# Kernel tuning notes

Measured on AMD Instinct MI355X. Metric: run time of the kernel, lower is better.

The kernel has to match this reference:

```python
import math
import jax, jax.numpy as jnp
import numpy as np

D_MODEL = 512
NHEAD = 8
D_HEAD = D_MODEL // NHEAD
ATTN_TEMP = 1.0
B, LQ, LK = 2, 2048, 4096


def _linear_params(key, d_in, d_out):
    kw, kb = jax.random.split(key)
    bound = 1.0 / math.sqrt(d_in)
    W = jax.random.uniform(kw, (d_out, d_in), jnp.float32, -bound, bound)
    b = jax.random.uniform(kb, (d_out,), jnp.float32, -bound, bound)
    return W, b


def setup_inputs() -> dict:
    key = jax.random.key(0)
    ks = jax.random.split(key, 8)
    q = jax.random.normal(ks[0], (B, LQ, D_MODEL), jnp.float32)
    kv = jax.random.normal(ks[1], (B, LK, D_MODEL), jnp.float32)
    key_gate = jax.random.uniform(ks[2], (B, LK), jnp.float32)
    key_mask = jax.random.randint(ks[3], (B, LK), 0, 2, jnp.int32)
    Wq, bq = _linear_params(ks[4], D_MODEL, D_MODEL)
    Wk, bk = _linear_params(ks[5], D_MODEL, D_MODEL)
    Wv, bv = _linear_params(ks[6], D_MODEL, D_MODEL)
    Wo, bo = _linear_params(ks[7], D_MODEL, D_MODEL)
    return {"q": q, "kv": kv, "key_gate": key_gate, "key_mask": key_mask,
            "Wq": Wq, "bq": bq, "Wk": Wk, "bk": bk,
            "Wv": Wv, "bv": bv, "Wo": Wo, "bo": bo}


def reference(q, kv, key_gate, key_mask, Wq, bq, Wk, bk, Wv, bv, Wo, bo):
    Bq, Lq, _ = q.shape
    _, Lk, _ = kv.shape
    # projections -> (B, H, L, Dh)
    qp = (q @ Wq.T + bq).reshape(Bq, Lq, NHEAD, D_HEAD).transpose(0, 2, 1, 3)
    kp = (kv @ Wk.T + bk).reshape(Bq, Lk, NHEAD, D_HEAD).transpose(0, 2, 1, 3)
    vp = (kv @ Wv.T + bv).reshape(Bq, Lk, NHEAD, D_HEAD).transpose(0, 2, 1, 3)
    # scores: (B, H, Lq, Lk)
    scores = jnp.einsum('bhqd,bhkd->bhqk', qp, kp) / (math.sqrt(D_HEAD) * ATTN_TEMP)
    log_gate = jnp.log(jnp.clip(key_gate, 1e-6, None))  # (B, Lk)
    scores = scores + log_gate[:, None, None, :]
    pad = (key_mask == 0)[:, None, None, :]
    scores = jnp.where(pad, -jnp.inf, scores)
    attn = jax.nn.softmax(scores, axis=-1)  # dropout is identity in eval
    out = jnp.einsum('bhqk,bhkd->bhqd', attn, vp)
    out = out.transpose(0, 2, 1, 3).reshape(Bq, Lq, D_MODEL)
    return out @ Wo.T + bo
```

## Files before the change

### kernel.cpp

```cpp
#include <hip/hip_runtime.h>
#include <hip/hip_bf16.h>


using bf16  = __hip_bfloat16;
using bf16x8 = __attribute__((ext_vector_type(8))) short;
using f32x4  = __attribute__((ext_vector_type(4))) float;

#define MFMA16(a, b, c) __builtin_amdgcn_mfma_f32_16x16x32_bf16((a), (b), (c), 0, 0, 0)

__device__ __forceinline__ bf16x8 load8(const bf16* p) {
    return *reinterpret_cast<const bf16x8*>(p);
}
__device__ __forceinline__ short f2bf(float x) {
    bf16 h = __float2bfloat16(x);
    return *reinterpret_cast<short*>(&h);
}

__global__ void cvt_x(const float* __restrict__ q, const float* __restrict__ kv,
                      bf16* __restrict__ qb, bf16* __restrict__ kvb) {
    int i = blockIdx.x * blockDim.x + threadIdx.x;
    const float* src; bf16* dst; int j;
    if (i < 524288) { src = q;  dst = qb;  j = i; }
    else            { src = kv; dst = kvb; j = i - 524288; }
    float4 v = reinterpret_cast<const float4*>(src)[j];
    ushort4 o;
    o.x = (unsigned short)f2bf(v.x);
    o.y = (unsigned short)f2bf(v.y);
    o.z = (unsigned short)f2bf(v.z);
    o.w = (unsigned short)f2bf(v.w);
    reinterpret_cast<ushort4*>(dst)[j] = o;
}

__global__ void cvt_w(const float* __restrict__ a, const float* __restrict__ b,
                      const float* __restrict__ c, const float* __restrict__ d,
                      bf16* __restrict__ oa, bf16* __restrict__ ob,
                      bf16* __restrict__ oc, bf16* __restrict__ od) {
    int i = blockIdx.x * blockDim.x + threadIdx.x;
    int t = i >> 16, j = i & 65535;
    const float* src = (t == 0) ? a : (t == 1) ? b : (t == 2) ? c : d;
    bf16*        dst = (t == 0) ? oa : (t == 1) ? ob : (t == 2) ? oc : od;
    float4 v = reinterpret_cast<const float4*>(src)[j];
    ushort4 o;
    o.x = (unsigned short)f2bf(v.x);
    o.y = (unsigned short)f2bf(v.y);
    o.z = (unsigned short)f2bf(v.z);
    o.w = (unsigned short)f2bf(v.w);
    reinterpret_cast<ushort4*>(dst)[j] = o;
}

__global__ void prep_gate_kernel(const float* __restrict__ gate,
                                 const int* __restrict__ mask,
                                 float* __restrict__ g, int n) {
    int i = blockIdx.x * blockDim.x + threadIdx.x;
    if (i < n) {
        float gv = fmaxf(gate[i], 1e-6f);
        g[i] = mask[i] ? logf(gv) : -1e30f;
    }
}

__device__ __forceinline__ void proj_body(const bf16* __restrict__ X,
                                          const bf16* __restrict__ W,
                                          const float* __restrict__ bias,
                                          void* __restrict__ Cout,
                                          int mode, int L, int mb, bf16* Ws) {
    const int tid  = threadIdx.x;
    const int wave = tid >> 6;
    const int lane = tid & 63;
    const int li   = lane & 15;
    const int quad = lane >> 4;
    const int n0   = blockIdx.x * 64;
    const int m0   = mb * 128 + wave * 32;

    f32x4 zero = {0.f, 0.f, 0.f, 0.f};
    f32x4 acc[2][4];
    for (int mt = 0; mt < 2; ++mt)
        for (int t = 0; t < 4; ++t) acc[mt][t] = zero;

    const bf16* x0 = X + (size_t)(m0 + li) * 512;
    const bf16* x1 = X + (size_t)(m0 + 16 + li) * 512;

    for (int p = 0; p < 2; ++p) {
        __syncthreads();
        for (int i = 0; i < 8; ++i) {
            const int c  = i * 256 + tid;
            const int cr = c >> 5;
            const int kc = (c & 31) * 8;
            *reinterpret_cast<bf16x8*>(&Ws[cr * 264 + kc]) =
                load8(W + (size_t)(n0 + cr) * 512 + p * 256 + kc);
        }
        __syncthreads();

        for (int k0 = 0; k0 < 256; k0 += 32) {
            bf16x8 a0 = load8(x0 + p * 256 + k0 + quad * 8);
            bf16x8 a1 = load8(x1 + p * 256 + k0 + quad * 8);
            for (int t = 0; t < 4; ++t) {
                bf16x8 w8 = load8(&Ws[(t * 16 + li) * 264 + k0 + quad * 8]);
                acc[0][t] = MFMA16(a0, w8, acc[0][t]);
                acc[1][t] = MFMA16(a1, w8, acc[1][t]);
            }
        }
    }

    for (int t = 0; t < 4; ++t) {
        const int col = n0 + t * 16 + li;
        const float bcol = bias[col];
        for (int mt = 0; mt < 2; ++mt) {
            for (int r = 0; r < 4; ++r) {
                const int row = m0 + mt * 16 + quad * 4 + r;
                const float v = acc[mt][t][r] + bcol;
                if (mode == 0) {
                    ((float*)Cout)[(size_t)row * 512 + col] = v;
                } else {
                    const int bb2 = row / L;
                    const int i   = row - bb2 * L;
                    const int hh  = col >> 6;
                    const int dh  = col & 63;
                    size_t idx;
                    if (mode == 1) idx = ((size_t)(bb2 * 8 + hh) * L + i) * 64 + dh;
                    else           idx = ((size_t)(bb2 * 8 + hh) * 64 + dh) * L + i;
                    ((bf16*)Cout)[idx] = __float2bfloat16(v);
                }
            }
        }
    }
}

__global__ void proj_qkv(const bf16* __restrict__ qb, const bf16* __restrict__ kvb,
                         const bf16* __restrict__ Wq, const float* __restrict__ bq,
                         const bf16* __restrict__ Wk, const float* __restrict__ bk,
                         const bf16* __restrict__ Wv, const float* __restrict__ bv,
                         bf16* __restrict__ qp, bf16* __restrict__ kp,
                         bf16* __restrict__ vpt) {
    __shared__ alignas(16) bf16 Ws[64 * 264];
    const int my = blockIdx.y;
    if (my < 32)      proj_body(qb,  Wq, bq, qp,  1, 2048, my,      Ws);
    else if (my < 96) proj_body(kvb, Wk, bk, kp,  1, 4096, my - 32, Ws);
    else              proj_body(kvb, Wv, bv, vpt, 2, 4096, my - 96, Ws);
}

__global__ void proj_o(const bf16* __restrict__ op, const bf16* __restrict__ Wo,
                       const float* __restrict__ bo, float* __restrict__ out) {
    __shared__ alignas(16) bf16 Ws[64 * 264];
    proj_body(op, Wo, bo, out, 0, 1, blockIdx.y, Ws);
}

#define PS 72
__global__ void attn_kernel(const bf16* __restrict__ qp, const bf16* __restrict__ kp,
                            const bf16* __restrict__ vpt, const float* __restrict__ g,
                            float* __restrict__ Opart, float* __restrict__ lpart) {
    __shared__ alignas(16) bf16 Kt[64 * PS];
    __shared__ alignas(16) bf16 Vt[64 * PS];
    __shared__ alignas(16) bf16 Pt[4 * 32 * PS];
    __shared__ float gs[64];

    const int tid  = threadIdx.x;
    const int wave = tid >> 6;
    const int lane = tid & 63;
    const int li   = lane & 15;
    const int quad = lane >> 4;

    const int bx = blockIdx.x;
    const int ks = bx & 3;
    const int qt = (bx >> 2) & 15;
    const int h  = (bx >> 6) & 7;
    const int b  = bx >> 9;
    const size_t bh = (size_t)(b * 8 + h);

    const bf16* qb0 = qp + (bh * 2048 + (size_t)qt * 128 + wave * 32 + li) * 64;
    bf16x8 aq[2][2];
    aq[0][0] = load8(qb0 + quad * 8);
    aq[0][1] = load8(qb0 + 32 + quad * 8);
    aq[1][0] = load8(qb0 + 16 * 64 + quad * 8);
    aq[1][1] = load8(qb0 + 16 * 64 + 32 + quad * 8);

    f32x4 zero = {0.f, 0.f, 0.f, 0.f};
    f32x4 o[2][4];
    for (int mt = 0; mt < 2; ++mt)
        for (int t = 0; t < 4; ++t) o[mt][t] = zero;
    float lsum[2][4] = {{0.f, 0.f, 0.f, 0.f}, {0.f, 0.f, 0.f, 0.f}};

    const bf16* ksrc  = kp  + bh * 4096 * 64;
    const bf16* vsrc  = vpt + bh * 64 * 4096;
    const float* gsrc = g + (size_t)b * 4096;

    bf16* PtW = &Pt[wave * 32 * PS];

    for (int kt = ks * 16; kt < ks * 16 + 16; ++kt) {
        {
            const int r0 = tid >> 3;
            const int cg = (tid & 7) * 8;
            const bf16* kst = ksrc + (size_t)kt * 64 * 64;
            *reinterpret_cast<bf16x8*>(&Kt[r0 * PS + cg])        = load8(kst + r0 * 64 + cg);
            *reinterpret_cast<bf16x8*>(&Kt[(r0 + 32) * PS + cg]) = load8(kst + (r0 + 32) * 64 + cg);
            const bf16* vs = vsrc + kt * 64;
            *reinterpret_cast<bf16x8*>(&Vt[r0 * PS + cg])        = load8(vs + (size_t)r0 * 4096 + cg);
            *reinterpret_cast<bf16x8*>(&Vt[(r0 + 32) * PS + cg]) = load8(vs + (size_t)(r0 + 32) * 4096 + cg);
            if (tid < 64) gs[tid] = gsrc[kt * 64 + tid];
        }
        __syncthreads();

        for (int t = 0; t < 4; ++t) {
            bf16x8 bk0 = load8(&Kt[(t * 16 + li) * PS + quad * 8]);
            bf16x8 bk1 = load8(&Kt[(t * 16 + li) * PS + 32 + quad * 8]);
            const float gv = gs[t * 16 + li];
            for (int mt = 0; mt < 2; ++mt) {
                f32x4 acc = zero;
                acc = MFMA16(aq[mt][0], bk0, acc);
                acc = MFMA16(aq[mt][1], bk1, acc);
                for (int r = 0; r < 4; ++r) {
                    const float p = __expf(acc[r] * 0.125f + gv);
                    lsum[mt][r] += p;
                    PtW[(mt * 16 + quad * 4 + r) * PS + t * 16 + li] = __float2bfloat16(p);
                }
            }
        }

        bf16x8 ap[2][2];
        ap[0][0] = load8(&PtW[li * PS + quad * 8]);
        ap[0][1] = load8(&PtW[li * PS + 32 + quad * 8]);
        ap[1][0] = load8(&PtW[(16 + li) * PS + quad * 8]);
        ap[1][1] = load8(&PtW[(16 + li) * PS + 32 + quad * 8]);
        for (int t = 0; t < 4; ++t) {
            bf16x8 bv0 = load8(&Vt[(t * 16 + li) * PS + quad * 8]);
            bf16x8 bv1 = load8(&Vt[(t * 16 + li) * PS + 32 + quad * 8]);
            for (int mt = 0; mt < 2; ++mt) {
                o[mt][t] = MFMA16(ap[mt][0], bv0, o[mt][t]);
                o[mt][t] = MFMA16(ap[mt][1], bv1, o[mt][t]);
            }
        }
        __syncthreads();
    }

    for (int off = 1; off < 16; off <<= 1)
        for (int mt = 0; mt < 2; ++mt)
            for (int r = 0; r < 4; ++r)
                lsum[mt][r] += __shfl_xor(lsum[mt][r], off);

    float* ob = Opart + ((size_t)bx * 128 + wave * 32) * 64;
    for (int mt = 0; mt < 2; ++mt)
        for (int t = 0; t < 4; ++t)
            for (int r = 0; r < 4; ++r)
                ob[(size_t)(mt * 16 + quad * 4 + r) * 64 + t * 16 + li] = o[mt][t][r];
    if (li == 0)
        for (int mt = 0; mt < 2; ++mt)
            for (int r = 0; r < 4; ++r)
                lpart[(size_t)bx * 128 + wave * 32 + mt * 16 + quad * 4 + r] = lsum[mt][r];
}

__global__ void attn_combine(const float* __restrict__ Opart,
                             const float* __restrict__ lpart,
                             bf16* __restrict__ op) {
    const int gidx = blockIdx.x * 256 + threadIdx.x;
    const int row  = gidx >> 2;
    const int c0   = (gidx & 3) * 16;
    const int b    = row >> 14;
    const int h    = (row >> 11) & 7;
    const int q    = row & 2047;
    const int qt   = q >> 7;
    const int r128 = q & 127;
    const int base = (((b * 8 + h) * 16) + qt) * 4;

    float acc[16];
    for (int j = 0; j < 16; ++j) acc[j] = 0.f;
    float L = 0.f;
    for (int s = 0; s < 4; ++s) {
        const float* src = Opart + ((size_t)(base + s) * 128 + r128) * 64 + c0;
        const float4 v0 = reinterpret_cast<const float4*>(src)[0];
        const float4 v1 = reinterpret_cast<const float4*>(src)[1];
        const float4 v2 = reinterpret_cast<const float4*>(src)[2];
        const float4 v3 = reinterpret_cast<const float4*>(src)[3];
        acc[0] += v0.x; acc[1] += v0.y; acc[2]  += v0.z; acc[3]  += v0.w;
        acc[4] += v1.x; acc[5] += v1.y; acc[6]  += v1.z; acc[7]  += v1.w;
        acc[8] += v2.x; acc[9] += v2.y; acc[10] += v2.z; acc[11] += v2.w;
        acc[12] += v3.x; acc[13] += v3.y; acc[14] += v3.z; acc[15] += v3.w;
        L += lpart[(size_t)(base + s) * 128 + r128];
    }
    const float invL = 1.0f / L;

    bf16* dst = op + ((size_t)b * 2048 + q) * 512 + h * 64 + c0;
    bf16x8 r0, r1;
    for (int j = 0; j < 8; ++j) {
        r0[j] = f2bf(acc[j] * invL);
        r1[j] = f2bf(acc[8 + j] * invL);
    }
    *reinterpret_cast<bf16x8*>(dst)     = r0;
    *reinterpret_cast<bf16x8*>(dst + 8) = r1;
}

extern "C" void kernel_launch(void* const* d_in, const int* in_sizes, int n_in,
                              void* d_out, int out_size, void* d_ws, size_t ws_size,
                              hipStream_t stream) {
    const float* q    = (const float*)d_in[0];
    const float* kv   = (const float*)d_in[1];
    const float* gate = (const float*)d_in[2];
    const int*   mask = (const int*)d_in[3];
    const float* Wq = (const float*)d_in[4];  const float* bq = (const float*)d_in[5];
    const float* Wk = (const float*)d_in[6];  const float* bk = (const float*)d_in[7];
    const float* Wv = (const float*)d_in[8];  const float* bv = (const float*)d_in[9];
    const float* Wo = (const float*)d_in[10]; const float* bo = (const float*)d_in[11];
    float* out = (float*)d_out;

    char* ws = (char*)d_ws;
    float* g   = (float*)ws;
    bf16* Wqb  = (bf16*)(ws + (1u  << 20));
    bf16* Wkb  = (bf16*)(ws + (1u  << 20) + (512u << 10));
    bf16* Wvb  = (bf16*)(ws + (2u  << 20));
    bf16* Wob  = (bf16*)(ws + (2u  << 20) + (512u << 10));
    bf16* qb   = (bf16*)(ws + (3u  << 20));
    bf16* kvb  = (bf16*)(ws + (7u  << 20));
    bf16* qp   = (bf16*)(ws + (15u << 20));
    bf16* kp   = (bf16*)(ws + (19u << 20));
    bf16* vpt  = (bf16*)(ws + (27u << 20));
    bf16* op   = (bf16*)(ws + (35u << 20));
    float* Opart = (float*)(ws + (39u << 20));
    float* lpart = (float*)(ws + (71u << 20));

    prep_gate_kernel<<<32, 256, 0, stream>>>(gate, mask, g, 2 * 4096);
    cvt_x<<<6144, 256, 0, stream>>>(q, kv, qb, kvb);
    cvt_w<<<1024, 256, 0, stream>>>(Wq, Wk, Wv, Wo, Wqb, Wkb, Wvb, Wob);

    proj_qkv<<<dim3(8, 160), 256, 0, stream>>>(qb, kvb, Wqb, bq, Wkb, bk,
                                               Wvb, bv, qp, kp, vpt);

    attn_kernel<<<1024, 256, 0, stream>>>(qp, kp, vpt, g, Opart, lpart);
    attn_combine<<<512, 256, 0, stream>>>(Opart, lpart, op);

    proj_o<<<dim3(8, 32), 256, 0, stream>>>(op, Wob, bo, out);
}
```

Measured before the change: 202.7 us.

## Fuse prep kernels, prefetch K/V tiles and weights, store partials in bf16

Merges the three preprocessing launches (activation cast, weight cast, gate log) into one kernel. The gate now uses log2 so the attention softmax can use exp2 with a folded scale. The attention loop register-prefetches the next K, V and gate tile while computing the current one. The projection prefetches the second weight half into registers, and the P scratch stride changes. Split-K partial outputs are stored in bf16 to halve combine traffic, which costs some accuracy in the partial sums.

```diff
diff --git a/kernel.cpp b/kernel.cpp
--- a/kernel.cpp
+++ b/kernel.cpp
@@ -8,6 +8,8 @@
 
 #define MFMA16(a, b, c) __builtin_amdgcn_mfma_f32_16x16x32_bf16((a), (b), (c), 0, 0, 0)
 
+#define SCALE_LOG2E 0.18033688011112042f
+
 __device__ __forceinline__ bf16x8 load8(const bf16* p) {
     return *reinterpret_cast<const bf16x8*>(p);
 }
@@ -15,46 +17,44 @@
     bf16 h = __float2bfloat16(x);
     return *reinterpret_cast<short*>(&h);
 }
-
-__global__ void cvt_x(const float* __restrict__ q, const float* __restrict__ kv,
-                      bf16* __restrict__ qb, bf16* __restrict__ kvb) {
-    int i = blockIdx.x * blockDim.x + threadIdx.x;
-    const float* src; bf16* dst; int j;
-    if (i < 524288) { src = q;  dst = qb;  j = i; }
-    else            { src = kv; dst = kvb; j = i - 524288; }
-    float4 v = reinterpret_cast<const float4*>(src)[j];
-    ushort4 o;
-    o.x = (unsigned short)f2bf(v.x);
-    o.y = (unsigned short)f2bf(v.y);
-    o.z = (unsigned short)f2bf(v.z);
-    o.w = (unsigned short)f2bf(v.w);
-    reinterpret_cast<ushort4*>(dst)[j] = o;
-}
-
-__global__ void cvt_w(const float* __restrict__ a, const float* __restrict__ b,
-                      const float* __restrict__ c, const float* __restrict__ d,
-                      bf16* __restrict__ oa, bf16* __restrict__ ob,
-                      bf16* __restrict__ oc, bf16* __restrict__ od) {
-    int i = blockIdx.x * blockDim.x + threadIdx.x;
-    int t = i >> 16, j = i & 65535;
-    const float* src = (t == 0) ? a : (t == 1) ? b : (t == 2) ? c : d;
-    bf16*        dst = (t == 0) ? oa : (t == 1) ? ob : (t == 2) ? oc : od;
-    float4 v = reinterpret_cast<const float4*>(src)[j];
-    ushort4 o;
-    o.x = (unsigned short)f2bf(v.x);
-    o.y = (unsigned short)f2bf(v.y);
-    o.z = (unsigned short)f2bf(v.z);
-    o.w = (unsigned short)f2bf(v.w);
-    reinterpret_cast<ushort4*>(dst)[j] = o;
-}
-
-__global__ void prep_gate_kernel(const float* __restrict__ gate,
-                                 const int* __restrict__ mask,
-                                 float* __restrict__ g, int n) {
-    int i = blockIdx.x * blockDim.x + threadIdx.x;
-    if (i < n) {
+__device__ __forceinline__ float bfb2f(short s) {
+    unsigned int u = ((unsigned int)(unsigned short)s) << 16;
+    return __builtin_bit_cast(float, u);
+}
+
+__global__ void prep_all(const float* __restrict__ q, const float* __restrict__ kv,
+                         const float* __restrict__ Wq, const float* __restrict__ Wk,
+                         const float* __restrict__ Wv, const float* __restrict__ Wo,
+                         const float* __restrict__ gate, const int* __restrict__ mask,
+                         bf16* __restrict__ qb, bf16* __restrict__ kvb,
+                         bf16* __restrict__ Wqb, bf16* __restrict__ Wkb,
+                         bf16* __restrict__ Wvb, bf16* __restrict__ Wob,
+                         float* __restrict__ g2) {
+    const int bid = blockIdx.x;
+    const int tid = threadIdx.x;
+    if (bid < 7168) {
+        const float* src; bf16* dst; int j;
+        if (bid < 6144) {
+            int i = bid * 256 + tid;
+            if (i < 524288) { src = q;  dst = qb;  j = i; }
+            else            { src = kv; dst = kvb; j = i - 524288; }
+        } else {
+            int i = (bid - 6144) * 256 + tid;
+            int t = i >> 16; j = i & 65535;
+            src = (t == 0) ? Wq : (t == 1) ? Wk : (t == 2) ? Wv : Wo;
+            dst = (t == 0) ? Wqb : (t == 1) ? Wkb : (t == 2) ? Wvb : Wob;
+        }
+        float4 v = reinterpret_cast<const float4*>(src)[j];
+        ushort4 o;
+        o.x = (unsigned short)f2bf(v.x);
+        o.y = (unsigned short)f2bf(v.y);
+        o.z = (unsigned short)f2bf(v.z);
+        o.w = (unsigned short)f2bf(v.w);
+        reinterpret_cast<ushort4*>(dst)[j] = o;
+    } else {
+        int i = (bid - 7168) * 256 + tid;
         float gv = fmaxf(gate[i], 1e-6f);
-        g[i] = mask[i] ? logf(gv) : -1e30f;
+        g2[i] = mask[i] ? log2f(gv) : -1e30f;
     }
 }
 
@@ -79,25 +79,49 @@
     const bf16* x0 = X + (size_t)(m0 + li) * 512;
     const bf16* x1 = X + (size_t)(m0 + 16 + li) * 512;
 
-    for (int p = 0; p < 2; ++p) {
-        __syncthreads();
-        for (int i = 0; i < 8; ++i) {
-            const int c  = i * 256 + tid;
-            const int cr = c >> 5;
-            const int kc = (c & 31) * 8;
-            *reinterpret_cast<bf16x8*>(&Ws[cr * 264 + kc]) =
-                load8(W + (size_t)(n0 + cr) * 512 + p * 256 + kc);
-        }
-        __syncthreads();
-
-        for (int k0 = 0; k0 < 256; k0 += 32) {
-            bf16x8 a0 = load8(x0 + p * 256 + k0 + quad * 8);
-            bf16x8 a1 = load8(x1 + p * 256 + k0 + quad * 8);
-            for (int t = 0; t < 4; ++t) {
-                bf16x8 w8 = load8(&Ws[(t * 16 + li) * 264 + k0 + quad * 8]);
-                acc[0][t] = MFMA16(a0, w8, acc[0][t]);
-                acc[1][t] = MFMA16(a1, w8, acc[1][t]);
-            }
+    for (int i = 0; i < 8; ++i) {
+        const int c  = i * 256 + tid;
+        const int cr = c >> 5;
+        const int kc = (c & 31) * 8;
+        *reinterpret_cast<bf16x8*>(&Ws[cr * 264 + kc]) =
+            load8(W + (size_t)(n0 + cr) * 512 + kc);
+    }
+    __syncthreads();
+
+    bf16x8 wpre[8];
+    for (int i = 0; i < 8; ++i) {
+        const int c  = i * 256 + tid;
+        const int cr = c >> 5;
+        const int kc = (c & 31) * 8;
+        wpre[i] = load8(W + (size_t)(n0 + cr) * 512 + 256 + kc);
+    }
+
+    for (int k0 = 0; k0 < 256; k0 += 32) {
+        bf16x8 a0 = load8(x0 + k0 + quad * 8);
+        bf16x8 a1 = load8(x1 + k0 + quad * 8);
+        for (int t = 0; t < 4; ++t) {
+            bf16x8 w8 = load8(&Ws[(t * 16 + li) * 264 + k0 + quad * 8]);
+            acc[0][t] = MFMA16(a0, w8, acc[0][t]);
+            acc[1][t] = MFMA16(a1, w8, acc[1][t]);
+        }
+    }
+    __syncthreads();
+
+    for (int i = 0; i < 8; ++i) {
+        const int c  = i * 256 + tid;
+        const int cr = c >> 5;
+        const int kc = (c & 31) * 8;
+        *reinterpret_cast<bf16x8*>(&Ws[cr * 264 + kc]) = wpre[i];
+    }
+    __syncthreads();
+
+    for (int k0 = 0; k0 < 256; k0 += 32) {
+        bf16x8 a0 = load8(x0 + 256 + k0 + quad * 8);
+        bf16x8 a1 = load8(x1 + 256 + k0 + quad * 8);
+        for (int t = 0; t < 4; ++t) {
+            bf16x8 w8 = load8(&Ws[(t * 16 + li) * 264 + k0 + quad * 8]);
+            acc[0][t] = MFMA16(a0, w8, acc[0][t]);
+            acc[1][t] = MFMA16(a1, w8, acc[1][t]);
         }
     }
 
@@ -144,13 +168,14 @@
     proj_body(op, Wo, bo, out, 0, 1, blockIdx.y, Ws);
 }
 
-#define PS 72
+#define PS  72
+#define PTS 68
 __global__ void attn_kernel(const bf16* __restrict__ qp, const bf16* __restrict__ kp,
-                            const bf16* __restrict__ vpt, const float* __restrict__ g,
-                            float* __restrict__ Opart, float* __restrict__ lpart) {
+                            const bf16* __restrict__ vpt, const float* __restrict__ g2,
+                            bf16* __restrict__ Opart, float* __restrict__ lpart) {
     __shared__ alignas(16) bf16 Kt[64 * PS];
     __shared__ alignas(16) bf16 Vt[64 * PS];
-    __shared__ alignas(16) bf16 Pt[4 * 32 * PS];
+    __shared__ alignas(16) bf16 Pt[4 * 32 * PTS];
     __shared__ float gs[64];
 
     const int tid  = threadIdx.x;
@@ -181,23 +206,42 @@
 
     const bf16* ksrc  = kp  + bh * 4096 * 64;
     const bf16* vsrc  = vpt + bh * 64 * 4096;
-    const float* gsrc = g + (size_t)b * 4096;
-
-    bf16* PtW = &Pt[wave * 32 * PS];
-
-    for (int kt = ks * 16; kt < ks * 16 + 16; ++kt) {
-        {
-            const int r0 = tid >> 3;
-            const int cg = (tid & 7) * 8;
-            const bf16* kst = ksrc + (size_t)kt * 64 * 64;
-            *reinterpret_cast<bf16x8*>(&Kt[r0 * PS + cg])        = load8(kst + r0 * 64 + cg);
-            *reinterpret_cast<bf16x8*>(&Kt[(r0 + 32) * PS + cg]) = load8(kst + (r0 + 32) * 64 + cg);
+    const float* gsrc = g2 + (size_t)b * 4096;
+
+    bf16* PtW = &Pt[wave * 32 * PTS];
+    const int r0 = tid >> 3;
+    const int cg = (tid & 7) * 8;
+
+    bf16x8 pk0, pk1, pv0, pv1;
+    float  pg = 0.f;
+    {
+        const bf16* kst = ksrc + (size_t)(ks * 16) * 4096;
+        pk0 = load8(kst + r0 * 64 + cg);
+        pk1 = load8(kst + (r0 + 32) * 64 + cg);
+        const bf16* vs = vsrc + (ks * 16) * 64;
+        pv0 = load8(vs + (size_t)r0 * 4096 + cg);
+        pv1 = load8(vs + (size_t)(r0 + 32) * 4096 + cg);
+        if (tid < 64) pg = gsrc[ks * 16 * 64 + tid];
+    }
+
+    for (int i = 0; i < 16; ++i) {
+        *reinterpret_cast<bf16x8*>(&Kt[r0 * PS + cg])        = pk0;
+        *reinterpret_cast<bf16x8*>(&Kt[(r0 + 32) * PS + cg]) = pk1;
+        *reinterpret_cast<bf16x8*>(&Vt[r0 * PS + cg])        = pv0;
+        *reinterpret_cast<bf16x8*>(&Vt[(r0 + 32) * PS + cg]) = pv1;
+        if (tid < 64) gs[tid] = pg;
+        __syncthreads();
+
+        if (i < 15) {
+            const int kt = ks * 16 + i + 1;
+            const bf16* kst = ksrc + (size_t)kt * 4096;
+            pk0 = load8(kst + r0 * 64 + cg);
+            pk1 = load8(kst + (r0 + 32) * 64 + cg);
             const bf16* vs = vsrc + kt * 64;
-            *reinterpret_cast<bf16x8*>(&Vt[r0 * PS + cg])        = load8(vs + (size_t)r0 * 4096 + cg);
-            *reinterpret_cast<bf16x8*>(&Vt[(r0 + 32) * PS + cg]) = load8(vs + (size_t)(r0 + 32) * 4096 + cg);
-            if (tid < 64) gs[tid] = gsrc[kt * 64 + tid];
-        }
-        __syncthreads();
+            pv0 = load8(vs + (size_t)r0 * 4096 + cg);
+            pv1 = load8(vs + (size_t)(r0 + 32) * 4096 + cg);
+            if (tid < 64) pg = gsrc[kt * 64 + tid];
+        }
 
         for (int t = 0; t < 4; ++t) {
             bf16x8 bk0 = load8(&Kt[(t * 16 + li) * PS + quad * 8]);
@@ -208,18 +252,18 @@
                 acc = MFMA16(aq[mt][0], bk0, acc);
                 acc = MFMA16(aq[mt][1], bk1, acc);
                 for (int r = 0; r < 4; ++r) {
-                    const float p = __expf(acc[r] * 0.125f + gv);
+                    const float p = exp2f(fmaf(acc[r], SCALE_LOG2E, gv));
                     lsum[mt][r] += p;
-                    PtW[(mt * 16 + quad * 4 + r) * PS + t * 16 + li] = __float2bfloat16(p);
+                    PtW[(mt * 16 + quad * 4 + r) * PTS + t * 16 + li] = __float2bfloat16(p);
                 }
             }
         }
 
         bf16x8 ap[2][2];
-        ap[0][0] = load8(&PtW[li * PS + quad * 8]);
-        ap[0][1] = load8(&PtW[li * PS + 32 + quad * 8]);
-        ap[1][0] = load8(&PtW[(16 + li) * PS + quad * 8]);
-        ap[1][1] = load8(&PtW[(16 + li) * PS + 32 + quad * 8]);
+        ap[0][0] = load8(&PtW[li * PTS + quad * 8]);
+        ap[0][1] = load8(&PtW[li * PTS + 32 + quad * 8]);
+        ap[1][0] = load8(&PtW[(16 + li) * PTS + quad * 8]);
+        ap[1][1] = load8(&PtW[(16 + li) * PTS + 32 + quad * 8]);
         for (int t = 0; t < 4; ++t) {
             bf16x8 bv0 = load8(&Vt[(t * 16 + li) * PS + quad * 8]);
             bf16x8 bv1 = load8(&Vt[(t * 16 + li) * PS + 32 + quad * 8]);
@@ -236,18 +280,19 @@
             for (int r = 0; r < 4; ++r)
                 lsum[mt][r] += __shfl_xor(lsum[mt][r], off);
 
-    float* ob = Opart + ((size_t)bx * 128 + wave * 32) * 64;
+    bf16* ob = Opart + ((size_t)bx * 128 + wave * 32) * 64;
     for (int mt = 0; mt < 2; ++mt)
         for (int t = 0; t < 4; ++t)
             for (int r = 0; r < 4; ++r)
-                ob[(size_t)(mt * 16 + quad * 4 + r) * 64 + t * 16 + li] = o[mt][t][r];
+                ob[(size_t)(mt * 16 + quad * 4 + r) * 64 + t * 16 + li] =
+                    __float2bfloat16(o[mt][t][r]);
     if (li == 0)
         for (int mt = 0; mt < 2; ++mt)
             for (int r = 0; r < 4; ++r)
                 lpart[(size_t)bx * 128 + wave * 32 + mt * 16 + quad * 4 + r] = lsum[mt][r];
 }
 
-__global__ void attn_combine(const float* __restrict__ Opart,
+__global__ void attn_combine(const bf16* __restrict__ Opart,
                              const float* __restrict__ lpart,
                              bf16* __restrict__ op) {
     const int gidx = blockIdx.x * 256 + threadIdx.x;
@@ -264,27 +309,25 @@
     for (int j = 0; j < 16; ++j) acc[j] = 0.f;
     float L = 0.f;
     for (int s = 0; s < 4; ++s) {
-        const float* src = Opart + ((size_t)(base + s) * 128 + r128) * 64 + c0;
-        const float4 v0 = reinterpret_cast<const float4*>(src)[0];
-        const float4 v1 = reinterpret_cast<const float4*>(src)[1];
-        const float4 v2 = reinterpret_cast<const float4*>(src)[2];
-        const float4 v3 = reinterpret_cast<const float4*>(src)[3];
-        acc[0] += v0.x; acc[1] += v0.y; acc[2]  += v0.z; acc[3]  += v0.w;
-        acc[4] += v1.x; acc[5] += v1.y; acc[6]  += v1.z; acc[7]  += v1.w;
-        acc[8] += v2.x; acc[9] += v2.y; acc[10] += v2.z; acc[11] += v2.w;
-        acc[12] += v3.x; acc[13] += v3.y; acc[14] += v3.z; acc[15] += v3.w;
+        const bf16* src = Opart + ((size_t)(base + s) * 128 + r128) * 64 + c0;
+        bf16x8 v0 = load8(src);
+        bf16x8 v1 = load8(src + 8);
+        for (int j = 0; j < 8; ++j) {
+            acc[j]     += bfb2f(v0[j]);
+            acc[8 + j] += bfb2f(v1[j]);
+        }
         L += lpart[(size_t)(base + s) * 128 + r128];
     }
     const float invL = 1.0f / L;
 
     bf16* dst = op + ((size_t)b * 2048 + q) * 512 + h * 64 + c0;
-    bf16x8 r0, r1;
+    bf16x8 o0, o1;
     for (int j = 0; j < 8; ++j) {
-        r0[j] = f2bf(acc[j] * invL);
-        r1[j] = f2bf(acc[8 + j] * invL);
-    }
-    *reinterpret_cast<bf16x8*>(dst)     = r0;
-    *reinterpret_cast<bf16x8*>(dst + 8) = r1;
+        o0[j] = f2bf(acc[j] * invL);
+        o1[j] = f2bf(acc[8 + j] * invL);
+    }
+    *reinterpret_cast<bf16x8*>(dst)     = o0;
+    *reinterpret_cast<bf16x8*>(dst + 8) = o1;
 }
 
 extern "C" void kernel_launch(void* const* d_in, const int* in_sizes, int n_in,
@@ -301,7 +344,7 @@
     float* out = (float*)d_out;
 
     char* ws = (char*)d_ws;
-    float* g   = (float*)ws;
+    float* g2  = (float*)ws;
     bf16* Wqb  = (bf16*)(ws + (1u  << 20));
     bf16* Wkb  = (bf16*)(ws + (1u  << 20) + (512u << 10));
     bf16* Wvb  = (bf16*)(ws + (2u  << 20));
@@ -312,18 +355,14 @@
     bf16* kp   = (bf16*)(ws + (19u << 20));
     bf16* vpt  = (bf16*)(ws + (27u << 20));
     bf16* op   = (bf16*)(ws + (35u << 20));
-    float* Opart = (float*)(ws + (39u << 20));
-    float* lpart = (float*)(ws + (71u << 20));
-
-    prep_gate_kernel<<<32, 256, 0, stream>>>(gate, mask, g, 2 * 4096);
-    cvt_x<<<6144, 256, 0, stream>>>(q, kv, qb, kvb);
-    cvt_w<<<1024, 256, 0, stream>>>(Wq, Wk, Wv, Wo, Wqb, Wkb, Wvb, Wob);
-
+    bf16* Opart = (bf16*)(ws + (39u << 20));
+    float* lpart = (float*)(ws + (55u << 20));
+
+    prep_all<<<7200, 256, 0, stream>>>(q, kv, Wq, Wk, Wv, Wo, gate, mask,
+                                       qb, kvb, Wqb, Wkb, Wvb, Wob, g2);
     proj_qkv<<<dim3(8, 160), 256, 0, stream>>>(qb, kvb, Wqb, bq, Wkb, bk,
                                                Wvb, bv, qp, kp, vpt);
-
-    attn_kernel<<<1024, 256, 0, stream>>>(qp, kp, vpt, g, Opart, lpart);
+    attn_kernel<<<1024, 256, 0, stream>>>(qp, kp, vpt, g2, Opart, lpart);
     attn_combine<<<512, 256, 0, stream>>>(Opart, lpart, op);
-
     proj_o<<<dim3(8, 32), 256, 0, stream>>>(op, Wob, bo, out);
 }
```

Measured after the change: 230.3 us. +13.7%, slower.
